# Performance work log

Hardware: AMD Instinct MI355X
Metric: run time of the kernel (lower is better)

## Reference

```python
import jax, jax.numpy as jnp
import numpy as np
from jax import lax

B, C, H, G = 128, 512, 14, 20  # batch, channels, feature-map size, num branches

# landmark indices for (point1, point2) of the 10 regions, and y-offset coefficients (x ruler)
_I1 = jnp.array([21, 18, 19, 41, 38, 49, 48, 51, 61, 56])
_I2 = jnp.array([22, 25, 24, 46, 43, 53, 54, 57, 63, 58])
_COEF = jnp.array([-0.5, -1.0 / 3.0, 1.0 / 3.0, 1.0, 0.0, 0.0, 0.0, 0.0, 0.0, 0.5], jnp.float32)


def process_landmarks(y):
    # y: [B,68,2] (x,y) pixel coords -> region_array [B,10,4] = (x1,y1,x2,y2)/16
    xl, yl = y[:, :, 0], y[:, :, 1]
    ruler = jnp.abs(xl[:, 39] - xl[:, 42])            # [B]
    off = ruler[:, None] * _COEF[None, :]             # [B,10]
    region = jnp.stack([xl[:, _I1], yl[:, _I1] + off, xl[:, _I2], yl[:, _I2] + off], axis=-1)
    return region / 16.0


def _crop(xi, cyi, cxi):
    # xi: [C,H,W]; 3x3 window centered at (cyi, cxi)
    z = jnp.asarray(0, cyi.dtype)
    return lax.dynamic_slice(xi, (z, cyi - 1, cxi - 1), (C, 3, 3))


def setup_inputs() -> dict:
    key = jax.random.key(0)
    ks = jax.random.split(key, 4)
    x = jax.random.normal(ks[0], (B, C, H, H), jnp.float32)
    y = jax.random.uniform(ks[1], (B, 68, 2), jnp.float32) * 224.0
    conv_w = jax.random.normal(ks[2], (G * C, C, 3, 3), jnp.float32) * 0.02  # grouped OIHW
    conv_b = jnp.zeros((G * C,), jnp.float32)
    fc_w = jax.random.normal(ks[3], (G, C * 36, 150), jnp.float32) * 0.01
    fc_b = jnp.zeros((G, 150), jnp.float32)
    return {"x": x, "y": y, "conv_w": conv_w, "conv_b": conv_b, "fc_w": fc_w, "fc_b": fc_b}


def reference(x, y, conv_w, conv_b, fc_w, fc_b):
    bsz = x.shape[0]
    pos = jnp.clip(process_landmarks(y).astype(jnp.int32), 1, 12)   # [B,10,4]
    cx = pos[:, :, jnp.array([0, 2])].reshape(bsz, G)               # [B,20] cols
    cy = pos[:, :, jnp.array([1, 3])].reshape(bsz, G)               # [B,20] rows
    crops = jax.vmap(jax.vmap(_crop, in_axes=(None, 0, 0)), in_axes=(0, 0, 0))(x, cy, cx)  # [B,20,C,3,3]
    new_input = crops.reshape(bsz, G * C, 3, 3)
    up = jax.image.resize(new_input, (bsz, G * C, 6, 6), method='bilinear')  # half-pixel, matches torch align_corners=False
    conv = lax.conv_general_dilated(up, conv_w, (1, 1), ((1, 1), (1, 1)),
                                    feature_group_count=G,
                                    dimension_numbers=('NCHW', 'OIHW', 'NCHW'))
    conv = jax.nn.relu(conv + conv_b[None, :, None, None])          # [B, G*C, 6, 6]
    feat = conv.reshape(bsz, G, C * 36)
    fc = jax.nn.relu(jnp.einsum('bgi,gio->bgo', feat, fc_w) + fc_b[None])  # [B,G,150]
    return fc.reshape(bsz, G * 150)
```

## Files before the change

### kernel.cpp

```cpp
#include <hip/hip_runtime.h>
#include <stdint.h>

#define B_  128
#define C_  512
#define G_  20
#define K2  4608
#define FCK 18432

typedef unsigned short u16;
typedef unsigned int   u32;
typedef __attribute__((ext_vector_type(8))) short  short8;
typedef __attribute__((ext_vector_type(4))) float  float4v;

__device__ __forceinline__ u16 f2bf(float f) {
  u32 u = __builtin_bit_cast(u32, f);
  u = (u + 0x7fffu + ((u >> 16) & 1u)) >> 16;
  return (u16)u;
}

__device__ __forceinline__ void load_lds16(const void* g, void* l) {
  __builtin_amdgcn_global_load_lds(
      (const __attribute__((address_space(1))) void*)(uintptr_t)g,
      (__attribute__((address_space(3))) void*)(uint32_t)(uintptr_t)l,
      16, 0, 0);
}

__global__ void k_pos(const float* __restrict__ y, int* __restrict__ cx, int* __restrict__ cy) {
  int b = blockIdx.x * blockDim.x + threadIdx.x;
  if (b >= B_) return;
  const int   I1[10] = {21,18,19,41,38,49,48,51,61,56};
  const int   I2[10] = {22,25,24,46,43,53,54,57,63,58};
  const float CF[10] = {-0.5f, -1.0f/3.0f, 1.0f/3.0f, 1.0f, 0.f,0.f,0.f,0.f,0.f, 0.5f};
  const float* yb = y + b * 136;
  float ruler = fabsf(yb[2*39] - yb[2*42]);
  for (int j = 0; j < 10; ++j) {
    float off = ruler * CF[j];
    float vx1 = yb[2*I1[j]];
    float vy1 = yb[2*I1[j]+1] + off;
    float vx2 = yb[2*I2[j]];
    float vy2 = yb[2*I2[j]+1] + off;
    int px1 = (int)(vx1 * 0.0625f); px1 = min(max(px1,1),12);
    int py1 = (int)(vy1 * 0.0625f); py1 = min(max(py1,1),12);
    int px2 = (int)(vx2 * 0.0625f); px2 = min(max(px2,1),12);
    int py2 = (int)(vy2 * 0.0625f); py2 = min(max(py2,1),12);
    cx[b*20 + 2*j]   = px1;  cx[b*20 + 2*j+1] = px2;
    cy[b*20 + 2*j]   = py1;  cy[b*20 + 2*j+1] = py2;
  }
}

__global__ void k_convw(const float* __restrict__ w, u16* __restrict__ wb) {
  int tid = blockIdx.x * 256 + threadIdx.x;
  int o = tid >> 9, ci = tid & 511;
  const float* src = w + (size_t)tid * 9;
  u16* dst = wb + (size_t)o * K2 + ci;
  #pragma unroll
  for (int t = 0; t < 9; ++t) dst[t*512] = f2bf(src[t]);
}

__global__ void __launch_bounds__(256) k_fcw(const float* __restrict__ fw, u16* __restrict__ wfcb) {
  __shared__ u16 tile[128 * 161];
  int chunk = blockIdx.x;
  int g     = blockIdx.y;
  int tid   = threadIdx.x;
  const float* src = fw + (size_t)g * FCK * 150 + (size_t)chunk * 128 * 150;
  #pragma unroll
  for (int it = 0; it < 75; ++it) {
    int f = it * 256 + tid;
    int il = f / 150, o = f - il * 150;
    tile[il * 161 + o] = f2bf(src[f]);
  }
  __syncthreads();
  size_t dstbase = (size_t)g * 160 * FCK + (size_t)chunk * 128;
  #pragma unroll
  for (int it = 0; it < 10; ++it) {
    int wi = it * 256 + tid;
    int o = wi >> 4, il8 = (wi & 15) * 8;
    u16 vals[8];
    if (o < 150) {
      #pragma unroll
      for (int j = 0; j < 8; ++j) vals[j] = tile[(il8 + j) * 161 + o];
    } else {
      #pragma unroll
      for (int j = 0; j < 8; ++j) vals[j] = 0;
    }
    *(short8*)(wfcb + dstbase + (size_t)o * FCK + il8) = *(short8*)vals;
  }
}

__global__ void __launch_bounds__(256) k_up3(const float* __restrict__ x,
                                             const int* __restrict__ cx,
                                             const int* __restrict__ cy,
                                             u16* __restrict__ up3) {
  __shared__ float crop[3][3][C_];
  int bg = blockIdx.x;
  int b = bg / 20, g = bg % 20;
  int X = cx[bg] - 1, Y = cy[bg] - 1;
  const float* xb = x + (size_t)b * (C_*14*14);
  int t = threadIdx.x;
  for (int it = 0; it < 6; ++it) {
    int idx = it*256 + t;
    int r = idx >> 9, ci = idx & 511;
    const float* srow = xb + ci*196 + (Y + r)*14 + X;
    crop[r][0][ci] = srow[0];
    crop[r][1][ci] = srow[1];
    crop[r][2][ci] = srow[2];
  }
  __syncthreads();
  const int   R0[6] = {0,0,0,1,1,1};
  const float WA[6] = {1.f, .75f, .25f, .75f, .25f, 0.f};
  u16* dstbase = up3 + ((size_t)g*B_ + b) * 64 * C_;
  for (int it = 0; it < 16; ++it) {
    int cidx = it*256 + t;
    int pp = cidx >> 6;
    int c8 = (cidx & 63) * 8;
    int ph = pp >> 3, pw = pp & 7;
    u16 outv[8];
    if (ph == 0 || ph == 7 || pw == 0 || pw == 7) {
      #pragma unroll
      for (int j = 0; j < 8; ++j) outv[j] = 0;
    } else {
      int oh = ph - 1, ow = pw - 1;
      int r0 = R0[oh]; float wy0 = WA[oh], wy1 = 1.f - WA[oh];
      int s0 = R0[ow]; float wx0 = WA[ow], wx1 = 1.f - WA[ow];
      #pragma unroll
      for (int j = 0; j < 8; ++j) {
        int ci = c8 + j;
        float v = wy0*(wx0*crop[r0][s0][ci]   + wx1*crop[r0][s0+1][ci])
                + wy1*(wx0*crop[r0+1][s0][ci] + wx1*crop[r0+1][s0+1][ci]);
        outv[j] = f2bf(v);
      }
    }
    *(short8*)(dstbase + (size_t)pp*C_ + c8) = *(short8*)outv;
  }
}

__global__ void __launch_bounds__(512) k_conv(const u16* __restrict__ wb,
                                              const u16* __restrict__ up3,
                                              const float* __restrict__ conv_b,
                                              u16* __restrict__ feat) {
  __shared__ __align__(16) u16 As[256*64];
  __shared__ __align__(16) u16 Bs[128*64];
  int bid = blockIdx.x;
  int lid = (bid & 7) * 180 + (bid >> 3);
  int mt = lid & 1;
  int nt = (lid >> 1) % 36;
  int g  = lid / 72;
  int tid = threadIdx.x;
  int lane = tid & 63, w = tid >> 6;
  int wr = w >> 1, wc = w & 1;
  int rl = lane >> 3, s = lane & 7;
  int l15 = lane & 15, l4 = lane >> 4;

  const u16* gA[4]; u16* lA[4];
  #pragma unroll
  for (int i = 0; i < 4; ++i) {
    int rA = w*32 + i*8 + rl;
    int c  = s ^ (rA & 7);
    gA[i] = wb + (size_t)(g*512 + mt*256 + rA) * K2 + c*8;
    lA[i] = (u16*)As + (w*32 + i*8) * 64;
  }
  const u16* gB[2]; u16* lB[2];
  #pragma unroll
  for (int i = 0; i < 2; ++i) {
    int rB = w*16 + i*8 + rl;
    int n  = nt*128 + rB;
    unsigned bb = (unsigned)n / 36u;
    unsigned pix = (unsigned)n % 36u;
    int pixA = (int)(pix/6u)*8 + (int)(pix%6u);
    int c = s ^ (rB & 7);
    gB[i] = up3 + (((size_t)g*B_ + bb)*64 + pixA) * C_ + c*8;
    lB[i] = (u16*)Bs + (w*16 + i*8) * 64;
  }

  float4v acc[4][4];
  #pragma unroll
  for (int mi = 0; mi < 4; ++mi)
    #pragma unroll
    for (int nj = 0; nj < 4; ++nj) acc[mi][nj] = (float4v){0.f,0.f,0.f,0.f};

  for (int step = 0; step < 72; ++step) {
    int t9  = step >> 3;
    int ci0 = (step & 7) * 64;
    size_t kofsA = (size_t)step * 64;
    size_t kofsB = (size_t)((t9/3)*8 + (t9%3)) * C_ + ci0;
    __syncthreads();
    #pragma unroll
    for (int i = 0; i < 4; ++i) load_lds16(gA[i] + kofsA, lA[i]);
    #pragma unroll
    for (int i = 0; i < 2; ++i) load_lds16(gB[i] + kofsB, lB[i]);
    __syncthreads();

    short8 a[4][2], bf[4][2];
    #pragma unroll
    for (int kb = 0; kb < 2; ++kb) {
      #pragma unroll
      for (int mi = 0; mi < 4; ++mi) {
        int row = wr*64 + mi*16 + l15;
        int cb  = (kb*64 + l4*16) ^ ((row & 7) << 4);
        a[mi][kb] = *(const short8*)((const char*)As + row*128 + cb);
      }
      #pragma unroll
      for (int nj = 0; nj < 4; ++nj) {
        int row = wc*64 + nj*16 + l15;
        int cb  = (kb*64 + l4*16) ^ ((row & 7) << 4);
        bf[nj][kb] = *(const short8*)((const char*)Bs + row*128 + cb);
      }
    }
    #pragma unroll
    for (int kb = 0; kb < 2; ++kb)
      #pragma unroll
      for (int mi = 0; mi < 4; ++mi)
        #pragma unroll
        for (int nj = 0; nj < 4; ++nj)
          acc[mi][nj] = __builtin_amdgcn_mfma_f32_16x16x32_bf16(
              a[mi][kb], bf[nj][kb], acc[mi][nj], 0, 0, 0);
  }

  float bias[4][4];
  #pragma unroll
  for (int mi = 0; mi < 4; ++mi)
    #pragma unroll
    for (int r = 0; r < 4; ++r)
      bias[mi][r] = conv_b[g*512 + mt*256 + wr*64 + mi*16 + l4*4 + r];
  #pragma unroll
  for (int nj = 0; nj < 4; ++nj) {
    int n = nt*128 + wc*64 + nj*16 + l15;
    unsigned bb = (unsigned)n / 36u;
    unsigned pix = (unsigned)n % 36u;
    size_t base = ((size_t)g*B_ + bb)*FCK + pix;
    #pragma unroll
    for (int mi = 0; mi < 4; ++mi)
      #pragma unroll
      for (int r = 0; r < 4; ++r) {
        int m = mt*256 + wr*64 + mi*16 + l4*4 + r;
        float v = fmaxf(acc[mi][nj][r] + bias[mi][r], 0.f);
        feat[base + (size_t)m*36] = f2bf(v);
      }
  }
}

__global__ void __launch_bounds__(256) k_fc(const u16* __restrict__ feat,
                                            const u16* __restrict__ wfcb,
                                            float* __restrict__ accum) {
  __shared__ __align__(16) u16 As[128*64];
  __shared__ __align__(16) u16 Bs[160*64];
  int sp = blockIdx.x;
  int g  = blockIdx.y;
  int tid = threadIdx.x;
  int lane = tid & 63, w = tid >> 6;
  int wr = w >> 1, wc = w & 1;
  int rl = lane >> 3, s = lane & 7;
  int l15 = lane & 15, l4 = lane >> 4;

  const u16* gA[4]; u16* lA[4];
  #pragma unroll
  for (int i = 0; i < 4; ++i) {
    int r = w*32 + i*8 + rl;
    int c = s ^ (r & 7);
    gA[i] = feat + ((size_t)g*B_ + r)*FCK + c*8;
    lA[i] = (u16*)As + (w*32 + i*8) * 64;
  }
  const u16* gB[5]; u16* lB[5];
  #pragma unroll
  for (int i = 0; i < 5; ++i) {
    int r = w*40 + i*8 + rl;
    int c = s ^ (r & 7);
    gB[i] = wfcb + ((size_t)(g*160 + r))*FCK + c*8;
    lB[i] = (u16*)Bs + (w*40 + i*8) * 64;
  }

  float4v acc[4][5];
  #pragma unroll
  for (int mi = 0; mi < 4; ++mi)
    #pragma unroll
    for (int nj = 0; nj < 5; ++nj) acc[mi][nj] = (float4v){0.f,0.f,0.f,0.f};

  size_t kbase = (size_t)sp * 1152;
  for (int stp = 0; stp < 18; ++stp) {
    size_t kofs = kbase + (size_t)stp * 64;
    __syncthreads();
    #pragma unroll
    for (int i = 0; i < 4; ++i) load_lds16(gA[i] + kofs, lA[i]);
    #pragma unroll
    for (int i = 0; i < 5; ++i) load_lds16(gB[i] + kofs, lB[i]);
    __syncthreads();

    short8 a[4][2], bf[5][2];
    #pragma unroll
    for (int kb = 0; kb < 2; ++kb) {
      #pragma unroll
      for (int mi = 0; mi < 4; ++mi) {
        int row = wr*64 + mi*16 + l15;
        int cb  = (kb*64 + l4*16) ^ ((row & 7) << 4);
        a[mi][kb] = *(const short8*)((const char*)As + row*128 + cb);
      }
      #pragma unroll
      for (int nj = 0; nj < 5; ++nj) {
        int row = wc*80 + nj*16 + l15;
        int cb  = (kb*64 + l4*16) ^ ((row & 7) << 4);
        bf[nj][kb] = *(const short8*)((const char*)Bs + row*128 + cb);
      }
    }
    #pragma unroll
    for (int kb = 0; kb < 2; ++kb)
      #pragma unroll
      for (int mi = 0; mi < 4; ++mi)
        #pragma unroll
        for (int nj = 0; nj < 5; ++nj)
          acc[mi][nj] = __builtin_amdgcn_mfma_f32_16x16x32_bf16(
              a[mi][kb], bf[nj][kb], acc[mi][nj], 0, 0, 0);
  }

  #pragma unroll
  for (int mi = 0; mi < 4; ++mi)
    #pragma unroll
    for (int r = 0; r < 4; ++r) {
      int brow = wr*64 + mi*16 + l4*4 + r;
      #pragma unroll
      for (int nj = 0; nj < 5; ++nj) {
        int o = wc*80 + nj*16 + l15;
        atomicAdd(&accum[((size_t)brow*20 + g)*160 + o], acc[mi][nj][r]);
      }
    }
}

__global__ void k_final(const float* __restrict__ accum, const float* __restrict__ fcb,
                        float* __restrict__ out) {
  int idx = blockIdx.x * 256 + threadIdx.x;
  if (idx >= B_*3000) return;
  unsigned b = (unsigned)idx / 3000u;
  unsigned rem = (unsigned)idx % 3000u;
  unsigned g = rem / 150u, o = rem % 150u;
  out[idx] = fmaxf(accum[((size_t)b*20 + g)*160 + o] + fcb[g*150 + o], 0.f);
}

extern "C" void kernel_launch(void* const* d_in, const int* in_sizes, int n_in,
                              void* d_out, int out_size, void* d_ws, size_t ws_size,
                              hipStream_t stream) {
  const float* x      = (const float*)d_in[0];
  const float* y      = (const float*)d_in[1];
  const float* conv_w = (const float*)d_in[2];
  const float* conv_b = (const float*)d_in[3];
  const float* fc_w   = (const float*)d_in[4];
  const float* fc_b   = (const float*)d_in[5];
  float* out = (float*)d_out;

  char* ws = (char*)d_ws;
  size_t off = 0;
  u16* Wb   = (u16*)(ws + off); off += (size_t)10240 * K2 * 2;
  u16* up3  = (u16*)(ws + off); off += (size_t)G_ * B_ * 64 * C_ * 2;
  u16* feat = (u16*)(ws + off); off += (size_t)G_ * B_ * FCK * 2;
  float* accum = (float*)(ws + off); off += (size_t)B_ * G_ * 160 * 4;
  int* cx = (int*)(ws + off); off += B_ * G_ * 4;
  int* cy = (int*)(ws + off); off += B_ * G_ * 4;
  u16* Wfcb = up3;

  k_pos<<<1, 128, 0, stream>>>(y, cx, cy);
  k_convw<<<(10240*512)/256, 256, 0, stream>>>(conv_w, Wb);
  k_up3<<<B_*G_, 256, 0, stream>>>(x, cx, cy, up3);
  hipMemsetAsync(accum, 0, (size_t)B_ * G_ * 160 * 4, stream);
  k_conv<<<1440, 512, 0, stream>>>(Wb, up3, conv_b, feat);
  k_fcw<<<dim3(144, 20), 256, 0, stream>>>(fc_w, Wfcb);
  k_fc<<<dim3(16, 20), 256, 0, stream>>>(feat, Wfcb, accum);
  k_final<<<(B_*3000 + 255)/256, 256, 0, stream>>>(accum, fc_b, out);
}
```

Measured before the change: 676.6 us.

## Triple-buffer conv GEMM LDS tiles with split-half prefetch and MFMA priority

The conv GEMM main loop moves from a single LDS buffer with two full barriers per step to a three-stage ring. Global-to-LDS loads for step t+2 are issued in two halves, interleaved with the two K-halves of MFMA work on step t. Explicit vmcnt waits, raw s_barrier and s_setprio are meant to hide global load latency behind compute. LDS use grows to about 144 KB per block, which may cut occupancy, and the hand-placed waitcnt logic is fragile.

```diff
diff --git a/kernel.cpp b/kernel.cpp
--- a/kernel.cpp
+++ b/kernel.cpp
@@ -138,8 +138,8 @@
                                               const u16* __restrict__ up3,
                                               const float* __restrict__ conv_b,
                                               u16* __restrict__ feat) {
-  __shared__ __align__(16) u16 As[256*64];
-  __shared__ __align__(16) u16 Bs[128*64];
+  __shared__ __align__(16) u16 As[3][256*64];
+  __shared__ __align__(16) u16 Bs[3][128*64];
   int bid = blockIdx.x;
   int lid = (bid & 7) * 180 + (bid >> 3);
   int mt = lid & 1;
@@ -151,15 +151,15 @@
   int rl = lane >> 3, s = lane & 7;
   int l15 = lane & 15, l4 = lane >> 4;
 
-  const u16* gA[4]; u16* lA[4];
+  const u16* gA[4]; int ofsA[4];
   #pragma unroll
   for (int i = 0; i < 4; ++i) {
     int rA = w*32 + i*8 + rl;
     int c  = s ^ (rA & 7);
     gA[i] = wb + (size_t)(g*512 + mt*256 + rA) * K2 + c*8;
-    lA[i] = (u16*)As + (w*32 + i*8) * 64;
-  }
-  const u16* gB[2]; u16* lB[2];
+    ofsA[i] = (w*32 + i*8) * 64;
+  }
+  const u16* gB[2]; int ofsB[2];
   #pragma unroll
   for (int i = 0; i < 2; ++i) {
     int rB = w*16 + i*8 + rl;
@@ -169,8 +169,27 @@
     int pixA = (int)(pix/6u)*8 + (int)(pix%6u);
     int c = s ^ (rB & 7);
     gB[i] = up3 + (((size_t)g*B_ + bb)*64 + pixA) * C_ + c*8;
-    lB[i] = (u16*)Bs + (w*16 + i*8) * 64;
-  }
+    ofsB[i] = (w*16 + i*8) * 64;
+  }
+
+  auto kofsB_of = [&](int st) -> size_t {
+    int t9 = st >> 3;
+    return (size_t)((t9/3)*8 + (t9%3)) * C_ + (size_t)(st & 7) * 64;
+  };
+  auto stage_h1 = [&](int st) {
+    int b3 = st % 3;
+    size_t kA = (size_t)st * 64, kB = kofsB_of(st);
+    load_lds16(gA[0] + kA, &As[b3][ofsA[0]]);
+    load_lds16(gA[1] + kA, &As[b3][ofsA[1]]);
+    load_lds16(gB[0] + kB, &Bs[b3][ofsB[0]]);
+  };
+  auto stage_h2 = [&](int st) {
+    int b3 = st % 3;
+    size_t kA = (size_t)st * 64, kB = kofsB_of(st);
+    load_lds16(gA[2] + kA, &As[b3][ofsA[2]]);
+    load_lds16(gA[3] + kA, &As[b3][ofsA[3]]);
+    load_lds16(gB[1] + kB, &Bs[b3][ofsB[1]]);
+  };
 
   float4v acc[4][4];
   #pragma unroll
@@ -178,42 +197,68 @@
     #pragma unroll
     for (int nj = 0; nj < 4; ++nj) acc[mi][nj] = (float4v){0.f,0.f,0.f,0.f};
 
-  for (int step = 0; step < 72; ++step) {
-    int t9  = step >> 3;
-    int ci0 = (step & 7) * 64;
-    size_t kofsA = (size_t)step * 64;
-    size_t kofsB = (size_t)((t9/3)*8 + (t9%3)) * C_ + ci0;
-    __syncthreads();
-    #pragma unroll
-    for (int i = 0; i < 4; ++i) load_lds16(gA[i] + kofsA, lA[i]);
-    #pragma unroll
-    for (int i = 0; i < 2; ++i) load_lds16(gB[i] + kofsB, lB[i]);
-    __syncthreads();
-
-    short8 a[4][2], bf[4][2];
-    #pragma unroll
-    for (int kb = 0; kb < 2; ++kb) {
+  stage_h1(0); stage_h2(0);
+  stage_h1(1); stage_h2(1);
+  asm volatile("s_waitcnt vmcnt(6)" ::: "memory");
+  __builtin_amdgcn_s_barrier();
+
+  for (int t = 0; t < 72; ++t) {
+    const char* curA = (const char*)As[t % 3];
+    const char* curB = (const char*)Bs[t % 3];
+    {
+      short8 a[4], bfr[4];
       #pragma unroll
       for (int mi = 0; mi < 4; ++mi) {
         int row = wr*64 + mi*16 + l15;
-        int cb  = (kb*64 + l4*16) ^ ((row & 7) << 4);
-        a[mi][kb] = *(const short8*)((const char*)As + row*128 + cb);
+        int cb  = (l4*16) ^ ((row & 7) << 4);
+        a[mi] = *(const short8*)(curA + row*128 + cb);
       }
       #pragma unroll
       for (int nj = 0; nj < 4; ++nj) {
         int row = wc*64 + nj*16 + l15;
-        int cb  = (kb*64 + l4*16) ^ ((row & 7) << 4);
-        bf[nj][kb] = *(const short8*)((const char*)Bs + row*128 + cb);
-      }
-    }
-    #pragma unroll
-    for (int kb = 0; kb < 2; ++kb)
+        int cb  = (l4*16) ^ ((row & 7) << 4);
+        bfr[nj] = *(const short8*)(curB + row*128 + cb);
+      }
+      if (t < 70) stage_h1(t + 2);
+      __builtin_amdgcn_s_barrier();
+      __builtin_amdgcn_s_setprio(1);
       #pragma unroll
       for (int mi = 0; mi < 4; ++mi)
         #pragma unroll
         for (int nj = 0; nj < 4; ++nj)
           acc[mi][nj] = __builtin_amdgcn_mfma_f32_16x16x32_bf16(
-              a[mi][kb], bf[nj][kb], acc[mi][nj], 0, 0, 0);
+              a[mi], bfr[nj], acc[mi][nj], 0, 0, 0);
+      __builtin_amdgcn_s_setprio(0);
+      __builtin_amdgcn_s_barrier();
+    }
+    {
+      short8 a[4], bfr[4];
+      #pragma unroll
+      for (int mi = 0; mi < 4; ++mi) {
+        int row = wr*64 + mi*16 + l15;
+        int cb  = (64 + l4*16) ^ ((row & 7) << 4);
+        a[mi] = *(const short8*)(curA + row*128 + cb);
+      }
+      #pragma unroll
+      for (int nj = 0; nj < 4; ++nj) {
+        int row = wc*64 + nj*16 + l15;
+        int cb  = (64 + l4*16) ^ ((row & 7) << 4);
+        bfr[nj] = *(const short8*)(curB + row*128 + cb);
+      }
+      if (t < 70) stage_h2(t + 2);
+      __builtin_amdgcn_s_barrier();
+      __builtin_amdgcn_s_setprio(1);
+      #pragma unroll
+      for (int mi = 0; mi < 4; ++mi)
+        #pragma unroll
+        for (int nj = 0; nj < 4; ++nj)
+          acc[mi][nj] = __builtin_amdgcn_mfma_f32_16x16x32_bf16(
+              a[mi], bfr[nj], acc[mi][nj], 0, 0, 0);
+      __builtin_amdgcn_s_setprio(0);
+      if (t < 70)       { asm volatile("s_waitcnt vmcnt(6)" ::: "memory"); }
+      else if (t == 70) { asm volatile("s_waitcnt vmcnt(0)" ::: "memory"); }
+      __builtin_amdgcn_s_barrier();
+    }
   }
 
   float bias[4][4];
```

Result: slower. 716.0 us (+5.8%).

## Double-buffer conv GEMM with 256x256 tiles and interleaved LDS prefetch

Applied to the files above, without the earlier changes.

Rewrites the grouped-conv implicit GEMM kernel to use 256x256 output tiles per block (8 waves in a 2x4 layout, 8x4 accumulators per wave), halving the grid. It double-buffers the A and B LDS tiles and issues the next K-step's global-to-LDS loads interleaved with MFMA quadrants, gating them with explicit vmcnt/lgkmcnt waits and raw barriers plus setprio around the MFMAs. The aim is to hide global load latency and raise data reuse per LDS byte. In exchange it uses 128 KB of LDS and more accumulator registers, which may limit occupancy despite the launch bound of 2, and the hand-placed waits are easy to get wrong.

```diff
diff --git a/kernel.cpp b/kernel.cpp
--- a/kernel.cpp
+++ b/kernel.cpp
@@ -24,6 +24,10 @@
       (__attribute__((address_space(3))) void*)(uint32_t)(uintptr_t)l,
       16, 0, 0);
 }
+
+#define BAR() __builtin_amdgcn_s_barrier()
+#define LGKM0() do { asm volatile("s_waitcnt lgkmcnt(0)" ::: "memory"); \
+                     __builtin_amdgcn_sched_barrier(0); } while (0)
 
 __global__ void k_pos(const float* __restrict__ y, int* __restrict__ cx, int* __restrict__ cy) {
   int b = blockIdx.x * blockDim.x + threadIdx.x;
@@ -134,105 +138,145 @@
   }
 }
 
-__global__ void __launch_bounds__(512) k_conv(const u16* __restrict__ wb,
-                                              const u16* __restrict__ up3,
-                                              const float* __restrict__ conv_b,
-                                              u16* __restrict__ feat) {
-  __shared__ __align__(16) u16 As[256*64];
-  __shared__ __align__(16) u16 Bs[128*64];
+__global__ void __launch_bounds__(512, 2) k_conv(const u16* __restrict__ wb,
+                                                 const u16* __restrict__ up3,
+                                                 const float* __restrict__ conv_b,
+                                                 u16* __restrict__ feat) {
+  __shared__ __align__(16) u16 As[2 * 256 * 64];
+  __shared__ __align__(16) u16 Bs[2 * 256 * 64];
   int bid = blockIdx.x;
-  int lid = (bid & 7) * 180 + (bid >> 3);
+  int lid = (bid & 7) * 90 + (bid >> 3);
   int mt = lid & 1;
-  int nt = (lid >> 1) % 36;
-  int g  = lid / 72;
+  int nt = (lid >> 1) % 18;
+  int g  = lid / 36;
   int tid = threadIdx.x;
-  int lane = tid & 63, w = tid >> 6;
-  int wr = w >> 1, wc = w & 1;
-  int rl = lane >> 3, s = lane & 7;
+  int lane = tid & 63;
+  int w = tid >> 6;
+  int wr = w >> 2, wc = w & 3;
   int l15 = lane & 15, l4 = lane >> 4;
 
-  const u16* gA[4]; u16* lA[4];
-  #pragma unroll
-  for (int i = 0; i < 4; ++i) {
-    int rA = w*32 + i*8 + rl;
-    int c  = s ^ (rA & 7);
-    gA[i] = wb + (size_t)(g*512 + mt*256 + rA) * K2 + c*8;
-    lA[i] = (u16*)As + (w*32 + i*8) * 64;
-  }
-  const u16* gB[2]; u16* lB[2];
-  #pragma unroll
-  for (int i = 0; i < 2; ++i) {
-    int rB = w*16 + i*8 + rl;
-    int n  = nt*128 + rB;
-    unsigned bb = (unsigned)n / 36u;
-    unsigned pix = (unsigned)n % 36u;
-    int pixA = (int)(pix/6u)*8 + (int)(pix%6u);
-    int c = s ^ (rB & 7);
-    gB[i] = up3 + (((size_t)g*B_ + bb)*64 + pixA) * C_ + c*8;
-    lB[i] = (u16*)Bs + (w*16 + i*8) * 64;
-  }
-
-  float4v acc[4][4];
-  #pragma unroll
-  for (int mi = 0; mi < 4; ++mi)
+  int rl0 = tid >> 3, sl0 = tid & 7;
+  const u16* srcA0 = wb + (size_t)(g*512 + mt*256 + rl0) * K2 + (sl0 ^ (rl0 & 7)) * 8;
+  const u16* srcB[2][2];
+  #pragma unroll
+  for (int h = 0; h < 2; ++h)
+    #pragma unroll
+    for (int j = 0; j < 2; ++j) {
+      int rl = j * 64 + rl0;
+      int n  = nt * 256 + h * 128 + rl;
+      unsigned bb = (unsigned)n / 36u;
+      unsigned pix = (unsigned)n % 36u;
+      int pixA = (int)(pix / 6u) * 8 + (int)(pix % 6u);
+      srcB[h][j] = up3 + (((size_t)g*B_ + bb)*64 + pixA) * C_ + (sl0 ^ (rl0 & 7)) * 8;
+    }
+
+  auto stageA = [&](int st, int h) {
+    if (st >= 72) return;
+    int db = st & 1;
+    size_t ko = (size_t)st * 64;
+    #pragma unroll
+    for (int j = 0; j < 2; ++j)
+      load_lds16(srcA0 + (size_t)(h*128 + j*64) * K2 + ko,
+                 (char*)As + db*32768 + h*16384 + (j*512 + tid)*16);
+  };
+  auto stageB = [&](int st, int h) {
+    if (st >= 72) return;
+    int db = st & 1;
+    int t9 = st >> 3;
+    size_t ko = (size_t)((t9/3)*8 + (t9%3)) * C_ + (size_t)(st & 7) * 64;
+    #pragma unroll
+    for (int j = 0; j < 2; ++j)
+      load_lds16(srcB[h][j] + ko,
+                 (char*)Bs + db*32768 + h*16384 + (j*512 + tid)*16);
+  };
+
+  auto ldfrag = [&](const char* base, int row, int kb) -> short8 {
+    int cb = (kb*64 + l4*16) ^ ((row & 7) << 4);
+    return *(const short8*)(base + row*128 + cb);
+  };
+
+  float4v acc[8][4];
+  #pragma unroll
+  for (int mi = 0; mi < 8; ++mi)
     #pragma unroll
     for (int nj = 0; nj < 4; ++nj) acc[mi][nj] = (float4v){0.f,0.f,0.f,0.f};
 
-  for (int step = 0; step < 72; ++step) {
-    int t9  = step >> 3;
-    int ci0 = (step & 7) * 64;
-    size_t kofsA = (size_t)step * 64;
-    size_t kofsB = (size_t)((t9/3)*8 + (t9%3)) * C_ + ci0;
-    __syncthreads();
-    #pragma unroll
-    for (int i = 0; i < 4; ++i) load_lds16(gA[i] + kofsA, lA[i]);
-    #pragma unroll
-    for (int i = 0; i < 2; ++i) load_lds16(gB[i] + kofsB, lB[i]);
-    __syncthreads();
-
-    short8 a[4][2], bf[4][2];
-    #pragma unroll
-    for (int kb = 0; kb < 2; ++kb) {
-      #pragma unroll
-      for (int mi = 0; mi < 4; ++mi) {
-        int row = wr*64 + mi*16 + l15;
-        int cb  = (kb*64 + l4*16) ^ ((row & 7) << 4);
-        a[mi][kb] = *(const short8*)((const char*)As + row*128 + cb);
-      }
-      #pragma unroll
-      for (int nj = 0; nj < 4; ++nj) {
-        int row = wc*64 + nj*16 + l15;
-        int cb  = (kb*64 + l4*16) ^ ((row & 7) << 4);
-        bf[nj][kb] = *(const short8*)((const char*)Bs + row*128 + cb);
-      }
-    }
-    #pragma unroll
-    for (int kb = 0; kb < 2; ++kb)
-      #pragma unroll
-      for (int mi = 0; mi < 4; ++mi)
-        #pragma unroll
-        for (int nj = 0; nj < 4; ++nj)
-          acc[mi][nj] = __builtin_amdgcn_mfma_f32_16x16x32_bf16(
-              a[mi][kb], bf[nj][kb], acc[mi][nj], 0, 0, 0);
-  }
-
-  float bias[4][4];
-  #pragma unroll
-  for (int mi = 0; mi < 4; ++mi)
+  stageB(0,0); stageB(0,1); stageA(0,0); stageA(0,1);
+  stageB(1,0); stageB(1,1); stageA(1,0); stageA(1,1);
+  asm volatile("s_waitcnt vmcnt(8)" ::: "memory");
+  BAR();
+
+  short8 aF[4][2], b01[2][2], b23[2][2];
+
+#define LDA_HALF(BASE, MH)                                        \
+  _Pragma("unroll") for (int mi = 0; mi < 4; ++mi)                \
+    _Pragma("unroll") for (int kb = 0; kb < 2; ++kb)              \
+      aF[mi][kb] = ldfrag(BASE, wr*128 + ((MH)*4 + mi)*16 + l15, kb);
+#define LDB_HALF(BASE, NH, DST)                                   \
+  _Pragma("unroll") for (int nj = 0; nj < 2; ++nj)                \
+    _Pragma("unroll") for (int kb = 0; kb < 2; ++kb)              \
+      DST[nj][kb] = ldfrag(BASE, wc*64 + ((NH)*2 + nj)*16 + l15, kb);
+#define MFMA_QUAD(BF, QM, QN)                                     \
+  __builtin_amdgcn_s_setprio(1);                                  \
+  _Pragma("unroll") for (int kb = 0; kb < 2; ++kb)                \
+    _Pragma("unroll") for (int mi = 0; mi < 4; ++mi)              \
+      _Pragma("unroll") for (int nj = 0; nj < 2; ++nj)            \
+        acc[(QM)*4+mi][(QN)*2+nj] = __builtin_amdgcn_mfma_f32_16x16x32_bf16( \
+            aF[mi][kb], BF[nj][kb], acc[(QM)*4+mi][(QN)*2+nj], 0, 0, 0);     \
+  __builtin_amdgcn_s_setprio(0);
+
+  for (int it = 0; it < 36; ++it) {
+    int t0 = 2 * it;
+    const char* A0 = (const char*)As;
+    const char* B0 = (const char*)Bs;
+    const char* A1 = (const char*)As + 32768;
+    const char* B1 = (const char*)Bs + 32768;
+    LDA_HALF(A0, 0); LDB_HALF(B0, 0, b01);
+    BAR(); LGKM0(); MFMA_QUAD(b01, 0, 0); BAR();
+    LDB_HALF(B0, 1, b23);
+    BAR(); LGKM0(); MFMA_QUAD(b23, 0, 1); BAR();
+    LDA_HALF(A0, 1);
+    stageB(t0 + 2, 0);
+    BAR(); LGKM0(); MFMA_QUAD(b01, 1, 0); BAR();
+    stageB(t0 + 2, 1); stageA(t0 + 2, 0);
+    BAR(); LGKM0(); MFMA_QUAD(b23, 1, 1);
+    if (it < 35) { asm volatile("s_waitcnt vmcnt(6)" ::: "memory"); }
+    else         { asm volatile("s_waitcnt vmcnt(0)" ::: "memory"); }
+    BAR();
+    LDA_HALF(A1, 0); LDB_HALF(B1, 0, b01);
+    stageA(t0 + 2, 1);
+    BAR(); LGKM0(); MFMA_QUAD(b01, 0, 0); BAR();
+    LDB_HALF(B1, 1, b23);
+    BAR(); LGKM0(); MFMA_QUAD(b23, 0, 1); BAR();
+    LDA_HALF(A1, 1);
+    stageB(t0 + 3, 0);
+    BAR(); LGKM0(); MFMA_QUAD(b01, 1, 0); BAR();
+    stageB(t0 + 3, 1); stageA(t0 + 3, 0); stageA(t0 + 3, 1);
+    BAR(); LGKM0(); MFMA_QUAD(b23, 1, 1);
+    asm volatile("s_waitcnt vmcnt(8)" ::: "memory");
+    BAR();
+  }
+#undef LDA_HALF
+#undef LDB_HALF
+#undef MFMA_QUAD
+
+  float bias[8][4];
+  #pragma unroll
+  for (int mi = 0; mi < 8; ++mi)
     #pragma unroll
     for (int r = 0; r < 4; ++r)
-      bias[mi][r] = conv_b[g*512 + mt*256 + wr*64 + mi*16 + l4*4 + r];
+      bias[mi][r] = conv_b[g*512 + mt*256 + wr*128 + mi*16 + l4*4 + r];
   #pragma unroll
   for (int nj = 0; nj < 4; ++nj) {
-    int n = nt*128 + wc*64 + nj*16 + l15;
+    int n = nt*256 + wc*64 + nj*16 + l15;
     unsigned bb = (unsigned)n / 36u;
     unsigned pix = (unsigned)n % 36u;
     size_t base = ((size_t)g*B_ + bb)*FCK + pix;
     #pragma unroll
-    for (int mi = 0; mi < 4; ++mi)
+    for (int mi = 0; mi < 8; ++mi)
       #pragma unroll
       for (int r = 0; r < 4; ++r) {
-        int m = mt*256 + wr*64 + mi*16 + l4*4 + r;
+        int m = mt*256 + wr*128 + mi*16 + l4*4 + r;
         float v = fmaxf(acc[mi][nj][r] + bias[mi][r], 0.f);
         feat[base + (size_t)m*36] = f2bf(v);
       }
@@ -359,7 +403,7 @@
   k_convw<<<(10240*512)/256, 256, 0, stream>>>(conv_w, Wb);
   k_up3<<<B_*G_, 256, 0, stream>>>(x, cx, cy, up3);
   hipMemsetAsync(accum, 0, (size_t)B_ * G_ * 160 * 4, stream);
-  k_conv<<<1440, 512, 0, stream>>>(Wb, up3, conv_b, feat);
+  k_conv<<<720, 512, 0, stream>>>(Wb, up3, conv_b, feat);
   k_fcw<<<dim3(144, 20), 256, 0, stream>>>(fc_w, Wfcb);
   k_fc<<<dim3(16, 20), 256, 0, stream>>>(feat, Wfcb, accum);
   k_final<<<(B_*3000 + 255)/256, 256, 0, stream>>>(accum, fc_b, out);
```

Measured after the change: 630.3 us. -6.8%, faster.
